# Kernel tuning notes

Hardware: AMD Instinct MI355X
Metric: run time of the kernel (lower is better)

The kernel has to match this reference:

```python
import jax, jax.numpy as jnp
import numpy as np
import math

B, S, D, H = 2, 4096, 128, 8

def setup_inputs() -> dict:
    key = jax.random.key(0)
    k1, k2, k3, k4 = jax.random.split(key, 4)
    x = jax.random.normal(k1, (B, S, D), dtype=jnp.float32)
    W_q = jax.random.normal(k2, (H, D, D), dtype=jnp.float32) * 0.02
    W_k = jax.random.normal(k3, (H, D, D), dtype=jnp.float32) * 0.02
    # nn.Linear weight: [out_features, in_features] = [D, D*H]
    W_o = jax.random.normal(k4, (D, D * H), dtype=jnp.float32) * (0.02 / math.sqrt(2 * 12))
    return {"x": x, "W_q": W_q, "W_k": W_k, "W_o": W_o}

def reference(x, W_q, W_k, W_o):
    b, s, d = x.shape
    h = W_q.shape[0]
    # Per-head projections of the same (repeated) input x.
    Q = jnp.einsum('bsd,hde->bhse', x, W_q)          # [B,H,S,D]
    K = jnp.einsum('bsd,hde->bhse', x, W_k)          # [B,H,S,D]
    scores = jnp.einsum('bhse,bhte->bhst', Q, K) / math.sqrt(d)  # [B,H,S,S]
    scores = jnp.clip(scores, -10.0, 10.0)
    causal = jnp.tril(jnp.ones((s, s), dtype=bool))  # [S,S]
    scores = jnp.where(causal[None, None], scores, -jnp.inf)
    attn = jax.nn.softmax(scores, axis=-1)           # dropout p=0 -> identity
    y = jnp.einsum('bhst,btd->bhsd', attn, x)        # V == x per head
    y = jnp.transpose(y, (0, 2, 1, 3)).reshape(b, s, h * d)  # [B,S,H*D]
    out = y @ W_o.T                                  # [B,S,D]
    return out
```

## Files before the change

kernel.cpp:

```cpp
#include <hip/hip_runtime.h>
#include <hip/hip_bf16.h>

typedef unsigned short u16;
typedef unsigned int u32;
typedef __attribute__((ext_vector_type(8))) short bf16x8;
typedef __attribute__((ext_vector_type(4))) float f32x4;
typedef __attribute__((ext_vector_type(16))) float f32x16;
typedef __attribute__((ext_vector_type(2))) unsigned int u32x2;
typedef __attribute__((ext_vector_type(4))) unsigned int u32x4;

#define S_LEN 4096
#define DHEAD 128
#define NHEAD 8
#define NBATCH 2

__device__ __forceinline__ u16 f2b(float f) {
  __hip_bfloat16 h = __float2bfloat16(f);
  return *(u16*)&h;
}

__device__ __forceinline__ f32x4 mfma16(bf16x8 a, bf16x8 b, f32x4 c) {
  return __builtin_amdgcn_mfma_f32_16x16x32_bf16(a, b, c, 0, 0, 0);
}
__device__ __forceinline__ f32x16 mfma32(bf16x8 a, bf16x8 b, f32x16 c) {
  return __builtin_amdgcn_mfma_f32_32x32x16_bf16(a, b, c, 0, 0, 0);
}

__device__ __forceinline__ f32x4 zero4() { f32x4 z = {0.f, 0.f, 0.f, 0.f}; return z; }

__device__ __forceinline__ u32 cvtpk(float lo, float hi) {
  u32 r;
  asm("v_cvt_pk_bf16_f32 %0, %1, %2" : "=v"(r) : "v"(lo), "v"(hi));
  return r;
}
__device__ __forceinline__ u32x2 pswap(u32 a, u32 b) {
  return __builtin_amdgcn_permlane32_swap(a, b, false, false);
}

__device__ __forceinline__ void gll16(const u16* g, u16* l) {
  __builtin_amdgcn_global_load_lds(
      (const __attribute__((address_space(1))) u32*)g,
      (__attribute__((address_space(3))) u32*)l, 16, 0, 0);
}

__global__ void k_conv_x(const float* __restrict__ x, u16* __restrict__ xb,
                         u16* __restrict__ VbF) {
  int idx = blockIdx.x * blockDim.x + threadIdx.x;
  float v = x[idx];
  u16 bv = f2b(v);
  xb[idx] = bv;
  int d = idx & 127;
  int bs = idx >> 7;
  int b = bs >> 12;
  int s = bs & 4095;
  int t64 = s >> 6, kh = (s >> 5) & 1, m2 = (s >> 4) & 1;
  int h5v = (s >> 3) & 1, j = s & 7;
  int db = d >> 5;
  int l = (d & 31) + 32 * h5v;
  int g = kh * 8 + m2 * 4 + db;
  VbF[(((size_t)b * 64 + t64) * 16 + g) * 512 + l * 8 + j] = bv;
}

__global__ void k_conv_w(const float* __restrict__ Wq, const float* __restrict__ Wk,
                         const float* __restrict__ Wo, u16* __restrict__ Wqt,
                         u16* __restrict__ Wkt, u16* __restrict__ WoB) {
  int idx = blockIdx.x * blockDim.x + threadIdx.x;
  int h = idx >> 14;
  int d = (idx >> 7) & 127;
  int e = idx & 127;
  int t = (h << 14) + (e << 7) + d;
  Wqt[t] = f2b(Wq[idx]);
  Wkt[t] = f2b(Wk[idx]);
  WoB[idx] = f2b(Wo[idx]);
}

__global__ __launch_bounds__(256) void k_proj(const u16* __restrict__ xb,
                                              const u16* __restrict__ Wqt,
                                              const u16* __restrict__ Wkt,
                                              u16* __restrict__ Qb, u16* __restrict__ KbF) {
  int wid = threadIdx.x >> 6;
  int lane = threadIdx.x & 63;
  int qt = blockIdx.x * 4 + wid;
  int h = blockIdx.y, z = blockIdx.z;
  int b = z >> 1, w = z & 1;
  int bh = b * NHEAD + h;
  int row16 = lane & 15, kgrp = lane >> 4;
  int sb = qt * 32;
  const u16* xp = xb + ((size_t)b * S_LEN + sb) * DHEAD;
  bf16x8 a[2][4];
#pragma unroll
  for (int r = 0; r < 2; ++r)
#pragma unroll
    for (int kc = 0; kc < 4; ++kc)
      a[r][kc] = *(const bf16x8*)(xp + (r * 16 + row16) * DHEAD + kc * 32 + kgrp * 8);

  const u16* Wt = (w == 0 ? Wqt : Wkt) + (size_t)h * DHEAD * DHEAD;
  f32x4 acc[2][8];
#pragma unroll
  for (int r = 0; r < 2; ++r)
#pragma unroll
    for (int nc = 0; nc < 8; ++nc) acc[r][nc] = zero4();
#pragma unroll
  for (int kc = 0; kc < 4; ++kc)
#pragma unroll
    for (int nc = 0; nc < 8; ++nc) {
      bf16x8 bw = *(const bf16x8*)(Wt + (nc * 16 + row16) * DHEAD + kc * 32 + kgrp * 8);
      acc[0][nc] = mfma16(a[0][kc], bw, acc[0][nc]);
      acc[1][nc] = mfma16(a[1][kc], bw, acc[1][nc]);
    }
  if (w == 0) {
    u16* Out = Qb + ((size_t)bh * S_LEN + sb) * DHEAD;
#pragma unroll
    for (int r = 0; r < 2; ++r)
#pragma unroll
      for (int nc = 0; nc < 8; ++nc)
#pragma unroll
        for (int i = 0; i < 4; ++i)
          Out[(size_t)(r * 16 + kgrp * 4 + i) * DHEAD + nc * 16 + row16] =
              f2b(acc[r][nc][i]);
  } else {
#pragma unroll
    for (int r = 0; r < 2; ++r)
#pragma unroll
      for (int nc = 0; nc < 8; ++nc)
#pragma unroll
        for (int i = 0; i < 4; ++i) {
          int key = sb + r * 16 + kgrp * 4 + i;
          int e = nc * 16 + row16;
          int t64 = key >> 6, kh = (key >> 5) & 1;
          int m = e >> 4;
          int l = (key & 31) + 32 * ((e >> 3) & 1);
          int j = e & 7;
          int f = kh * 8 + m;
          KbF[(((size_t)bh * 64 + t64) * 16 + f) * 512 + l * 8 + j] = f2b(acc[r][nc][i]);
        }
  }
}

__global__ __launch_bounds__(512) void k_attn(const u16* __restrict__ Qb,
                                              const u16* __restrict__ KbF,
                                              const u16* __restrict__ VbF,
                                              u16* __restrict__ Yb) {
  int p = blockIdx.x;
  int xcd = p & 7;
  int j2 = p >> 3;
  int bh = xcd + (j2 >= 16 ? 8 : 0);
  int qpj = j2 & 15;
  int b = bh >> 3, h = bh & 7;

  int tid = threadIdx.x;
  int wid = tid >> 6;
  int lane = tid & 63;
  int qr = wid >> 1;
  int kh = wid & 1;
  int l31 = lane & 31, h5 = lane >> 5;

  __shared__ __align__(16) u16 Klds[2][8192];
  __shared__ __align__(16) float Scr[8192];
  __shared__ float rsbuf[2][4][32];

  const u16* Kbase = KbF + (size_t)bh * 64 * 16 * 512;
  const u16* Vbase = VbF + (size_t)b * 64 * 16 * 512;

  auto issue = [&](int k0, int buf) {
    const u16* Ks = Kbase + (size_t)(k0 >> 6) * 16 * 512;
#pragma unroll
    for (int fi = 0; fi < 2; ++fi) {
      int f = wid * 2 + fi;
      gll16(Ks + f * 512 + lane * 8, &Klds[buf][f * 512]);
    }
  };
  auto vload = [&](bf16x8 (&dst)[8], int k0) {
    const u16* Vs = Vbase + ((size_t)(k0 >> 6) * 16 + kh * 8) * 512 + lane * 8;
#pragma unroll
    for (int g = 0; g < 8; ++g) dst[g] = *(const bf16x8*)(Vs + g * 512);
  };

  const float c2 = 0.12754274816295166f;
  const float clip2 = 14.426950408889634f;

  auto runSeg = [&](int qblk) {
    int qb0 = qblk * 128;
    int qw = qb0 + qr * 32;
    int qrow = qw + l31;
    const u16* Qp = Qb + ((size_t)bh * S_LEN + qw) * DHEAD;

    bf16x8 bq[8];
#pragma unroll
    for (int m = 0; m < 8; ++m)
      bq[m] = *(const bf16x8*)(Qp + (size_t)l31 * DHEAD + m * 16 + h5 * 8);

    f32x16 y0, y1, y2, y3;
#pragma unroll
    for (int i = 0; i < 16; ++i) { y0[i] = 0.f; y1[i] = 0.f; y2[i] = 0.f; y3[i] = 0.f; }
    float rs = 0.f;

    bf16x8 vA[8], vB[8];

    auto tilecomp = [&](int buf, int k0, bf16x8 (&vc)[8], bf16x8 (&vn)[8], int kn0) {
      f32x16 sc;
#pragma unroll
      for (int i = 0; i < 16; ++i) sc[i] = 0.f;
      __builtin_amdgcn_s_setprio(1);
#pragma unroll
      for (int m = 0; m < 8; ++m) {
        bf16x8 kf = *(const bf16x8*)&Klds[buf][((kh * 8 + m) * 512) + lane * 8];
        sc = mfma32(kf, bq[m], sc);
      }
      __builtin_amdgcn_s_setprio(0);
      vload(vn, kn0);

      float pf[16];
      int kb = k0 + kh * 32 + h5 * 4;
      bool nomask = (k0 + kh * 32 + 31) <= qw;
      if (nomask) {
#pragma unroll
        for (int reg = 0; reg < 16; ++reg) {
          float v = __builtin_amdgcn_fmed3f(sc[reg] * c2, -clip2, clip2);
          float pc = __builtin_amdgcn_exp2f(v);
          rs += pc;
          pf[reg] = pc;
        }
      } else {
#pragma unroll
        for (int reg = 0; reg < 16; ++reg) {
          int key = kb + (reg & 3) + 8 * (reg >> 2);
          float v = __builtin_amdgcn_fmed3f(sc[reg] * c2, -clip2, clip2);
          float pc = __builtin_amdgcn_exp2f(v);
          pc = (key > qrow) ? 0.0f : pc;
          rs += pc;
          pf[reg] = pc;
        }
      }
      u32 cv0 = cvtpk(pf[0], pf[1]), cv1 = cvtpk(pf[2], pf[3]);
      u32 cv2 = cvtpk(pf[4], pf[5]), cv3 = cvtpk(pf[6], pf[7]);
      u32 cv4 = cvtpk(pf[8], pf[9]), cv5 = cvtpk(pf[10], pf[11]);
      u32 cv6 = cvtpk(pf[12], pf[13]), cv7 = cvtpk(pf[14], pf[15]);
      u32x2 s0 = pswap(cv0, cv2);
      u32x2 s1 = pswap(cv1, cv3);
      u32x2 s2 = pswap(cv4, cv6);
      u32x2 s3 = pswap(cv5, cv7);
      u32x4 pa0u = {s0.x, s1.x, s0.y, s1.y};
      u32x4 pa1u = {s2.x, s3.x, s2.y, s3.y};
      bf16x8 pa0 = __builtin_bit_cast(bf16x8, pa0u);
      bf16x8 pa1 = __builtin_bit_cast(bf16x8, pa1u);
      __builtin_amdgcn_s_setprio(1);
      y0 = mfma32(pa0, vc[0], y0);
      y0 = mfma32(pa1, vc[4], y0);
      y1 = mfma32(pa0, vc[1], y1);
      y1 = mfma32(pa1, vc[5], y1);
      y2 = mfma32(pa0, vc[2], y2);
      y2 = mfma32(pa1, vc[6], y2);
      y3 = mfma32(pa0, vc[3], y3);
      y3 = mfma32(pa1, vc[7], y3);
      __builtin_amdgcn_s_setprio(0);
    };

    int NT = 2 * qblk + 2;
    issue(0, 0);
    vload(vA, 0);
    __syncthreads();
    for (int t = 0; t < NT; t += 2) {
      int k0 = t * 64;
      issue(k0 + 64, 1);
      tilecomp(0, k0, vA, vB, k0 + 64);
      __syncthreads();
      int k1 = k0 + 64;
      bool more = (t + 2 < NT);
      if (more) issue(k1 + 64, 0);
      tilecomp(1, k1, vB, vA, more ? k1 + 64 : k1);
      __syncthreads();
    }

    rs += __shfl_xor(rs, 32, 64);

#pragma unroll
    for (int pr = 0; pr < 2; ++pr) {
      float* scr = Scr + (qr >> 1) * 4096;
      if ((qr & 1) == pr && kh == 1) {
#pragma unroll
        for (int db = 0; db < 4; ++db) {
          const f32x16& yv = (db == 0) ? y0 : (db == 1) ? y1 : (db == 2) ? y2 : y3;
#pragma unroll
          for (int r4 = 0; r4 < 4; ++r4) {
            f32x4 ch = {yv[r4 * 4 + 0], yv[r4 * 4 + 1], yv[r4 * 4 + 2], yv[r4 * 4 + 3]};
            *(f32x4*)&scr[((db * 4 + r4) * 64 + lane) * 4] = ch;
          }
        }
        if (lane < 32) rsbuf[1][qr][lane] = rs;
      }
      __syncthreads();
      if ((qr & 1) == pr && kh == 0) {
        float rs2 = rs + rsbuf[1][qr][l31];
        float inv = 1.0f / rs2;
        if (lane < 32) rsbuf[0][qr][lane] = inv;
#pragma unroll
        for (int db = 0; db < 4; ++db) {
          f32x16& yv = (db == 0) ? y0 : (db == 1) ? y1 : (db == 2) ? y2 : y3;
#pragma unroll
          for (int r4 = 0; r4 < 4; ++r4) {
            f32x4 ch = *(const f32x4*)&scr[((db * 4 + r4) * 64 + lane) * 4];
#pragma unroll
            for (int k = 0; k < 4; ++k) yv[r4 * 4 + k] += ch[k];
          }
        }
        u16* Yp = Yb + ((size_t)b * S_LEN + qw) * (NHEAD * DHEAD) + h * DHEAD;
#pragma unroll
        for (int db = 0; db < 4; ++db) {
          const f32x16& yv = (db == 0) ? y0 : (db == 1) ? y1 : (db == 2) ? y2 : y3;
#pragma unroll
          for (int reg = 0; reg < 16; ++reg) {
            int qp2 = (reg & 3) + 8 * (reg >> 2) + 4 * h5;
            float rv = rsbuf[0][qr][qp2];
            Yp[(size_t)qp2 * (NHEAD * DHEAD) + db * 32 + l31] = f2b(yv[reg] * rv);
          }
        }
      }
      __syncthreads();
    }
  };

  runSeg(31 - qpj);
  runSeg(qpj);
}

__global__ __launch_bounds__(256) void k_oproj(const u16* __restrict__ Yb,
                                               const u16* __restrict__ WoB,
                                               float* __restrict__ out) {
  int wid = threadIdx.x >> 6;
  int lane = threadIdx.x & 63;
  int mb = (blockIdx.x * 4 + wid) * 32 + blockIdx.y * 16;
  int nb = blockIdx.z * 64;
  int row16 = lane & 15, kgrp = lane >> 4;
  f32x4 acc[4];
#pragma unroll
  for (int nc = 0; nc < 4; ++nc) acc[nc] = zero4();
#pragma unroll 4
  for (int kc = 0; kc < 32; ++kc) {
    bf16x8 a0 = *(const bf16x8*)(Yb + (size_t)(mb + row16) * 1024 + kc * 32 + kgrp * 8);
#pragma unroll
    for (int nc = 0; nc < 4; ++nc) {
      bf16x8 bw =
          *(const bf16x8*)(WoB + (size_t)(nb + nc * 16 + row16) * 1024 + kc * 32 + kgrp * 8);
      acc[nc] = mfma16(a0, bw, acc[nc]);
    }
  }
#pragma unroll
  for (int nc = 0; nc < 4; ++nc)
#pragma unroll
    for (int i = 0; i < 4; ++i)
      out[(size_t)(mb + kgrp * 4 + i) * DHEAD + nb + nc * 16 + row16] = acc[nc][i];
}

extern "C" void kernel_launch(void* const* d_in, const int* in_sizes, int n_in,
                              void* d_out, int out_size, void* d_ws, size_t ws_size,
                              hipStream_t stream) {
  const float* x = (const float*)d_in[0];
  const float* Wq = (const float*)d_in[1];
  const float* Wk = (const float*)d_in[2];
  const float* Wo = (const float*)d_in[3];
  float* out = (float*)d_out;

  char* ws = (char*)d_ws;
  size_t off = 0;
  auto alloc = [&](size_t bytes) -> void* {
    void* p = ws + off;
    off += (bytes + 255) & ~(size_t)255;
    return p;
  };
  const size_t nx = (size_t)NBATCH * S_LEN * DHEAD;
  const size_t nqk = (size_t)NBATCH * NHEAD * S_LEN * DHEAD;
  u16* xb = (u16*)alloc(nx * 2);
  u16* VbF = (u16*)alloc(nx * 2);
  u16* Wqt = (u16*)alloc((size_t)NHEAD * DHEAD * DHEAD * 2);
  u16* Wkt = (u16*)alloc((size_t)NHEAD * DHEAD * DHEAD * 2);
  u16* WoB = (u16*)alloc((size_t)DHEAD * NHEAD * DHEAD * 2);
  u16* Qb = (u16*)alloc(nqk * 2);
  u16* KbF = (u16*)alloc(nqk * 2);
  u16* Yb = (u16*)alloc(nqk * 2);
  (void)ws_size;

  k_conv_x<<<dim3(nx / 256), dim3(256), 0, stream>>>(x, xb, VbF);
  k_conv_w<<<dim3(131072 / 256), dim3(256), 0, stream>>>(Wq, Wk, Wo, Wqt, Wkt, WoB);
  k_proj<<<dim3(S_LEN / 32 / 4, NHEAD, 2 * NBATCH), dim3(256), 0, stream>>>(xb, Wqt, Wkt, Qb, KbF);
  k_attn<<<dim3(256), dim3(512), 0, stream>>>(Qb, KbF, VbF, Yb);
  k_oproj<<<dim3((NBATCH * S_LEN) / 32 / 4, 2, 2), dim3(256), 0, stream>>>(Yb, WoB, out);
}
```

Before: 158.4 us.

## Deepen K ring to four LDS buffers, halve barriers, single-phase reduction

Replaces the two K buffers plus separate scratch with a unified four-slot LDS ring, prefetching two K tiles ahead so only one barrier is needed per pair of tiles. V register loads are hoisted out of the tile compute and issued earlier. The final cross-wave reduction reuses the ring memory so all four row groups reduce in one phase, removing two barriers. This relies on the async LDS loads completing by the barrier, and it changes register live ranges.

```diff
diff --git a/kernel.cpp b/kernel.cpp
--- a/kernel.cpp
+++ b/kernel.cpp
@@ -155,8 +155,7 @@
   int kh = wid & 1;
   int l31 = lane & 31, h5 = lane >> 5;
 
-  __shared__ __align__(16) u16 Klds[2][8192];
-  __shared__ __align__(16) float Scr[8192];
+  __shared__ __align__(16) u16 SMEM[4][8192];
   __shared__ float rsbuf[2][4][32];
 
   const u16* Kbase = KbF + (size_t)bh * 64 * 16 * 512;
@@ -167,7 +166,7 @@
 #pragma unroll
     for (int fi = 0; fi < 2; ++fi) {
       int f = wid * 2 + fi;
-      gll16(Ks + f * 512 + lane * 8, &Klds[buf][f * 512]);
+      gll16(Ks + f * 512 + lane * 8, &SMEM[buf][f * 512]);
     }
   };
   auto vload = [&](bf16x8 (&dst)[8], int k0) {
@@ -197,18 +196,17 @@
 
     bf16x8 vA[8], vB[8];
 
-    auto tilecomp = [&](int buf, int k0, bf16x8 (&vc)[8], bf16x8 (&vn)[8], int kn0) {
+    auto tilecomp = [&](int buf, int k0, bf16x8 (&vc)[8]) {
       f32x16 sc;
 #pragma unroll
       for (int i = 0; i < 16; ++i) sc[i] = 0.f;
       __builtin_amdgcn_s_setprio(1);
 #pragma unroll
       for (int m = 0; m < 8; ++m) {
-        bf16x8 kf = *(const bf16x8*)&Klds[buf][((kh * 8 + m) * 512) + lane * 8];
+        bf16x8 kf = *(const bf16x8*)&SMEM[buf][((kh * 8 + m) * 512) + lane * 8];
         sc = mfma32(kf, bq[m], sc);
       }
       __builtin_amdgcn_s_setprio(0);
-      vload(vn, kn0);
 
       float pf[16];
       int kb = k0 + kh * 32 + h5 * 4;
@@ -258,66 +256,63 @@
 
     int NT = 2 * qblk + 2;
     issue(0, 0);
+    issue(64, 1);
     vload(vA, 0);
     __syncthreads();
     for (int t = 0; t < NT; t += 2) {
       int k0 = t * 64;
-      issue(k0 + 64, 1);
-      tilecomp(0, k0, vA, vB, k0 + 64);
+      vload(vB, k0 + 64);
+      if (t + 2 < NT) issue(k0 + 128, (t + 2) & 3);
+      if (t + 3 < NT) issue(k0 + 192, (t + 3) & 3);
+      tilecomp(t & 3, k0, vA);
+      if (t + 2 < NT) vload(vA, k0 + 128);
+      tilecomp((t + 1) & 3, k0 + 64, vB);
       __syncthreads();
-      int k1 = k0 + 64;
-      bool more = (t + 2 < NT);
-      if (more) issue(k1 + 64, 0);
-      tilecomp(1, k1, vB, vA, more ? k1 + 64 : k1);
-      __syncthreads();
     }
 
     rs += __shfl_xor(rs, 32, 64);
 
-#pragma unroll
-    for (int pr = 0; pr < 2; ++pr) {
-      float* scr = Scr + (qr >> 1) * 4096;
-      if ((qr & 1) == pr && kh == 1) {
-#pragma unroll
-        for (int db = 0; db < 4; ++db) {
-          const f32x16& yv = (db == 0) ? y0 : (db == 1) ? y1 : (db == 2) ? y2 : y3;
-#pragma unroll
-          for (int r4 = 0; r4 < 4; ++r4) {
-            f32x4 ch = {yv[r4 * 4 + 0], yv[r4 * 4 + 1], yv[r4 * 4 + 2], yv[r4 * 4 + 3]};
-            *(f32x4*)&scr[((db * 4 + r4) * 64 + lane) * 4] = ch;
-          }
-        }
-        if (lane < 32) rsbuf[1][qr][lane] = rs;
-      }
-      __syncthreads();
-      if ((qr & 1) == pr && kh == 0) {
-        float rs2 = rs + rsbuf[1][qr][l31];
-        float inv = 1.0f / rs2;
-        if (lane < 32) rsbuf[0][qr][lane] = inv;
-#pragma unroll
-        for (int db = 0; db < 4; ++db) {
-          f32x16& yv = (db == 0) ? y0 : (db == 1) ? y1 : (db == 2) ? y2 : y3;
-#pragma unroll
-          for (int r4 = 0; r4 < 4; ++r4) {
-            f32x4 ch = *(const f32x4*)&scr[((db * 4 + r4) * 64 + lane) * 4];
-#pragma unroll
-            for (int k = 0; k < 4; ++k) yv[r4 * 4 + k] += ch[k];
-          }
-        }
-        u16* Yp = Yb + ((size_t)b * S_LEN + qw) * (NHEAD * DHEAD) + h * DHEAD;
-#pragma unroll
-        for (int db = 0; db < 4; ++db) {
-          const f32x16& yv = (db == 0) ? y0 : (db == 1) ? y1 : (db == 2) ? y2 : y3;
-#pragma unroll
-          for (int reg = 0; reg < 16; ++reg) {
-            int qp2 = (reg & 3) + 8 * (reg >> 2) + 4 * h5;
-            float rv = rsbuf[0][qr][qp2];
-            Yp[(size_t)qp2 * (NHEAD * DHEAD) + db * 32 + l31] = f2b(yv[reg] * rv);
-          }
-        }
-      }
-      __syncthreads();
-    }
+    float* scr = (float*)&SMEM[0][0] + qr * 4096;
+    if (kh == 1) {
+#pragma unroll
+      for (int db = 0; db < 4; ++db) {
+        const f32x16& yv = (db == 0) ? y0 : (db == 1) ? y1 : (db == 2) ? y2 : y3;
+#pragma unroll
+        for (int r4 = 0; r4 < 4; ++r4) {
+          f32x4 ch = {yv[r4 * 4 + 0], yv[r4 * 4 + 1], yv[r4 * 4 + 2], yv[r4 * 4 + 3]};
+          *(f32x4*)&scr[((db * 4 + r4) * 64 + lane) * 4] = ch;
+        }
+      }
+      if (lane < 32) rsbuf[1][qr][lane] = rs;
+    }
+    __syncthreads();
+    if (kh == 0) {
+      float rs2 = rs + rsbuf[1][qr][l31];
+      float inv = 1.0f / rs2;
+      if (lane < 32) rsbuf[0][qr][lane] = inv;
+#pragma unroll
+      for (int db = 0; db < 4; ++db) {
+        f32x16& yv = (db == 0) ? y0 : (db == 1) ? y1 : (db == 2) ? y2 : y3;
+#pragma unroll
+        for (int r4 = 0; r4 < 4; ++r4) {
+          f32x4 ch = *(const f32x4*)&scr[((db * 4 + r4) * 64 + lane) * 4];
+#pragma unroll
+          for (int k = 0; k < 4; ++k) yv[r4 * 4 + k] += ch[k];
+        }
+      }
+      u16* Yp = Yb + ((size_t)b * S_LEN + qw) * (NHEAD * DHEAD) + h * DHEAD;
+#pragma unroll
+      for (int db = 0; db < 4; ++db) {
+        const f32x16& yv = (db == 0) ? y0 : (db == 1) ? y1 : (db == 2) ? y2 : y3;
+#pragma unroll
+        for (int reg = 0; reg < 16; ++reg) {
+          int qp2 = (reg & 3) + 8 * (reg >> 2) + 4 * h5;
+          float rv = rsbuf[0][qr][qp2];
+          Yp[(size_t)qp2 * (NHEAD * DHEAD) + db * 32 + l31] = f2b(yv[reg] * rv);
+        }
+      }
+    }
+    __syncthreads();
   };
 
   runSeg(31 - qpj);
```

Result: faster. 145.9 us (-7.9%).
